# Performance work log

Measured on AMD Instinct MI355X. Metric: run time of the kernel, lower is better.

Reference implementation:

```python
import jax, jax.numpy as jnp
import numpy as np

N = 50000
E = 800000
IN_C, HID, OUT_C, HEADS = 128, 16, 64, 4
NEG_SLOPE = 0.2


def _gat_conv(x, src, dst, W, a_src, a_dst, b, heads, concat):
    # x: [N, Fin]; W: [Fin, heads*Fout]; a_src/a_dst: [heads, Fout]; b: [out]
    n = x.shape[0]
    h = (x @ W).reshape(n, heads, -1)                      # [N, H, F]
    alpha_s = jnp.einsum('nhf,hf->nh', h, a_src)           # [N, H]
    alpha_d = jnp.einsum('nhf,hf->nh', h, a_dst)
    e = jax.nn.leaky_relu(alpha_s[src] + alpha_d[dst], NEG_SLOPE)  # [E, H]
    m = jax.ops.segment_max(e, dst, num_segments=n)        # per-dest max (self-loops ensure nonempty)
    w = jnp.exp(e - m[dst])
    denom = jax.ops.segment_sum(w, dst, num_segments=n)
    alpha = w / (denom[dst] + 1e-16)                       # [E, H] segment softmax
    out = jax.ops.segment_sum(h[src] * alpha[:, :, None], dst, num_segments=n)  # [N, H, F]
    out = out.reshape(n, -1) if concat else out.mean(axis=1)
    return out + b


def setup_inputs() -> dict:
    key = jax.random.key(0)
    ks = jax.random.split(key, 16)
    x = jax.random.normal(ks[0], (N, IN_C), dtype=jnp.float32)
    edge_index = jax.random.randint(ks[1], (2, E), 0, N, dtype=jnp.int64)
    s = 0.1
    d = {'x': x, 'edge_index': edge_index}
    # layer 0: in=128 -> heads=4, F=16
    d['W0'] = jax.random.normal(ks[2], (IN_C, HEADS * HID), dtype=jnp.float32) * s
    d['as0'] = jax.random.normal(ks[3], (HEADS, HID), dtype=jnp.float32) * s
    d['ad0'] = jax.random.normal(ks[4], (HEADS, HID), dtype=jnp.float32) * s
    d['b0'] = jnp.zeros((HEADS * HID,), dtype=jnp.float32)
    # layer 1: in=64 -> heads=4, F=16
    d['W1'] = jax.random.normal(ks[5], (HEADS * HID, HEADS * HID), dtype=jnp.float32) * s
    d['as1'] = jax.random.normal(ks[6], (HEADS, HID), dtype=jnp.float32) * s
    d['ad1'] = jax.random.normal(ks[7], (HEADS, HID), dtype=jnp.float32) * s
    d['b1'] = jnp.zeros((HEADS * HID,), dtype=jnp.float32)
    # layer 2: in=64 -> heads=1, F=64, concat=False
    d['W2'] = jax.random.normal(ks[8], (HEADS * HID, OUT_C), dtype=jnp.float32) * s
    d['as2'] = jax.random.normal(ks[9], (1, OUT_C), dtype=jnp.float32) * s
    d['ad2'] = jax.random.normal(ks[10], (1, OUT_C), dtype=jnp.float32) * s
    d['b2'] = jnp.zeros((OUT_C,), dtype=jnp.float32)
    return d


def reference(x, edge_index, W0, as0, ad0, b0, W1, as1, ad1, b1, W2, as2, ad2, b2):
    loops = jnp.arange(N, dtype=edge_index.dtype)
    src = jnp.concatenate([edge_index[0], loops])  # PyG add_self_loops=True
    dst = jnp.concatenate([edge_index[1], loops])
    h = _gat_conv(x, src, dst, W0, as0, ad0, b0, HEADS, True)
    h = jax.nn.elu(h)
    h = _gat_conv(h, src, dst, W1, as1, ad1, b1, HEADS, True)
    h = jax.nn.elu(h)
    return _gat_conv(h, src, dst, W2, as2, ad2, b2, 1, False)
```

## Files before the change

### kernel.cpp

```cpp
#include <hip/hip_runtime.h>
#include <hip/hip_bf16.h>
#include <math.h>


#define NEG_SLOPE 0.2f
#define L1_CHUNK 4096


__global__ __launch_bounds__(256) void k_l1hist(
    const int* __restrict__ idx, int* __restrict__ ghist, int E, int etot) {
    __shared__ int h[256];
    const int t = threadIdx.x;
    h[t] = 0;
    __syncthreads();
    const int base = blockIdx.x * L1_CHUNK;
    for (int i = t; i < L1_CHUNK; i += 256) {
        int e = base + i;
        if (e >= etot) break;
        int dst = (e < E) ? idx[E + e] : (e - E);
        atomicAdd(&h[dst >> 8], 1);
    }
    __syncthreads();
    if (h[t]) atomicAdd(&ghist[t], h[t]);
}

__global__ __launch_bounds__(256) void k_scan256(
    const int* __restrict__ ghist, int* __restrict__ goff, int* __restrict__ gcur) {
    __shared__ int sc[256];
    const int t = threadIdx.x;
    int v = ghist[t];
    sc[t] = v;
    __syncthreads();
    for (int o = 1; o < 256; o <<= 1) {
        int x = (t >= o) ? sc[t - o] : 0;
        __syncthreads();
        sc[t] += x;
        __syncthreads();
    }
    int excl = sc[t] - v;
    goff[t] = excl;
    gcur[t] = excl;
    if (t == 255) goff[256] = sc[255];
}

__global__ __launch_bounds__(256) void k_l1scatter(
    const int* __restrict__ idx, int* __restrict__ gcur,
    unsigned long long* __restrict__ buf, int E, int etot) {
    __shared__ int h[256];
    __shared__ int lbase[256];
    const int t = threadIdx.x;
    h[t] = 0;
    __syncthreads();
    const int base = blockIdx.x * L1_CHUNK;
    for (int i = t; i < L1_CHUNK; i += 256) {
        int e = base + i;
        if (e >= etot) break;
        int dst = (e < E) ? idx[E + e] : (e - E);
        atomicAdd(&h[dst >> 8], 1);
    }
    __syncthreads();
    lbase[t] = h[t] ? atomicAdd(&gcur[t], h[t]) : 0;
    __syncthreads();
    h[t] = lbase[t];
    __syncthreads();
    for (int i = t; i < L1_CHUNK; i += 256) {
        int e = base + i;
        if (e >= etot) break;
        int dst, src;
        if (e < E) { dst = idx[E + e]; src = idx[e]; }
        else       { dst = src = e - E; }
        int pos = atomicAdd(&h[dst >> 8], 1);
        buf[pos] = ((unsigned long long)(unsigned)dst << 32) | (unsigned)src;
    }
}

__global__ __launch_bounds__(256) void k_l2build(
    const unsigned long long* __restrict__ buf, const int* __restrict__ goff,
    int* __restrict__ off, int* __restrict__ csr, int n, int etot) {
    __shared__ int sc[256];
    __shared__ int lcur[256];
    const int b = blockIdx.x, t = threadIdx.x;
    const int lo = goff[b], hi = goff[b + 1];
    sc[t] = 0;
    __syncthreads();
    for (int p = lo + t; p < hi; p += 256) {
        int dst = (int)(buf[p] >> 32);
        atomicAdd(&sc[dst & 255], 1);
    }
    __syncthreads();
    int v = sc[t];
    __syncthreads();
    sc[t] = v;
    __syncthreads();
    for (int o = 1; o < 256; o <<= 1) {
        int x = (t >= o) ? sc[t - o] : 0;
        __syncthreads();
        sc[t] += x;
        __syncthreads();
    }
    int excl = sc[t] - v;
    const int d = b * 256 + t;
    if (d < n) off[d] = lo + excl;
    lcur[t] = lo + excl;
    __syncthreads();
    for (int p = lo + t; p < hi; p += 256) {
        unsigned long long e = buf[p];
        int dst = (int)(e >> 32);
        int src = (int)(e & 0xffffffffu);
        int pos = atomicAdd(&lcur[dst & 255], 1);
        csr[pos] = src;
    }
    if (b == 0 && t == 0) off[n] = etot;
}


template <int H>
__device__ __forceinline__ float4 agg_node(
    const float* __restrict__ h, const float* __restrict__ asb,
    const float* __restrict__ adb, const int* __restrict__ off,
    const int* __restrict__ csr, int node, int q, int c4) {
    const int head = (H == 1) ? 0 : (c4 >> 2);
    const float ad_n = adb[node * H + head];
    const int b = off[node], e = off[node + 1];
    float den = 0.f;
    float4 acc = {0.f, 0.f, 0.f, 0.f};
    int p = b + q;
    int s_cur = 0; float as_cur = 0.f;
    if (p < e) { s_cur = csr[p]; as_cur = asb[s_cur * H + head]; }
    while (p < e) {
        const int pn = p + 4;
        int s_nxt = 0; float as_nxt = 0.f;
        if (pn < e) { s_nxt = csr[pn]; as_nxt = asb[s_nxt * H + head]; }
        float ev = as_cur + ad_n;
        ev = ev > 0.f ? ev : NEG_SLOPE * ev;
        float wv = __expf(ev);
        const float4 hv = *(const float4*)(h + (size_t)s_cur * 64 + c4 * 4);
        den += wv;
        acc.x = fmaf(wv, hv.x, acc.x);
        acc.y = fmaf(wv, hv.y, acc.y);
        acc.z = fmaf(wv, hv.z, acc.z);
        acc.w = fmaf(wv, hv.w, acc.w);
        p = pn; s_cur = s_nxt; as_cur = as_nxt;
    }
    den += __shfl_xor(den, 16); den += __shfl_xor(den, 32);
    acc.x += __shfl_xor(acc.x, 16); acc.x += __shfl_xor(acc.x, 32);
    acc.y += __shfl_xor(acc.y, 16); acc.y += __shfl_xor(acc.y, 32);
    acc.z += __shfl_xor(acc.z, 16); acc.z += __shfl_xor(acc.z, 32);
    acc.w += __shfl_xor(acc.w, 16); acc.w += __shfl_xor(acc.w, 32);
    float inv = 1.f / (den + 1e-16f);
    return make_float4(acc.x * inv, acc.y * inv, acc.z * inv, acc.w * inv);
}

template <int K, int H, int F>
__global__ __launch_bounds__(256) void k_gemm_alpha(
    const float* __restrict__ x, const float* __restrict__ W,
    const float* __restrict__ a_s, const float* __restrict__ a_d,
    float* __restrict__ h, float* __restrict__ as_o, float* __restrict__ ad_o,
    int n) {
    __shared__ float xs[16][K];
    const int tid = threadIdx.x;
    const int base = blockIdx.x * 16;
    int rows = n - base; if (rows > 16) rows = 16;
    const int kv = K / 4;
    for (int i = tid; i < rows * kv; i += 256) {
        int r = i / kv, c = i - r * kv;
        ((float4*)&xs[r][0])[c] = ((const float4*)(x + (size_t)(base + r) * K))[c];
    }
    __syncthreads();
    const int w = tid >> 6, lane = tid & 63;
    const int node0 = base + w * 4;
    float acc0 = 0.f, acc1 = 0.f, acc2 = 0.f, acc3 = 0.f;
    #pragma unroll 4
    for (int k = 0; k < K; ++k) {
        float wv = W[k * 64 + lane];
        acc0 = fmaf(xs[w * 4 + 0][k], wv, acc0);
        acc1 = fmaf(xs[w * 4 + 1][k], wv, acc1);
        acc2 = fmaf(xs[w * 4 + 2][k], wv, acc2);
        acc3 = fmaf(xs[w * 4 + 3][k], wv, acc3);
    }
    const int head = (H == 1) ? 0 : (lane >> 4);
    const int f = (H == 1) ? lane : (lane & (F - 1));
    const float asv = a_s[head * F + f];
    const float adv = a_d[head * F + f];
    float accs[4] = {acc0, acc1, acc2, acc3};
    #pragma unroll
    for (int j = 0; j < 4; ++j) {
        int node = node0 + j;
        if (node >= n) break;
        h[(size_t)node * 64 + lane] = accs[j];
        float vs = accs[j] * asv;
        float vd = accs[j] * adv;
        #pragma unroll
        for (int o = F >> 1; o > 0; o >>= 1) {
            vs += __shfl_xor(vs, o);
            vd += __shfl_xor(vd, o);
        }
        if (f == 0) {
            as_o[node * H + head] = vs;
            ad_o[node * H + head] = vd;
        }
    }
}

template <int HA, int HG, int FG>
__global__ __launch_bounds__(256) void k_agg_gemm(
    const float* __restrict__ h_in, const float* __restrict__ asb_in,
    const float* __restrict__ adb_in, const int* __restrict__ off,
    const int* __restrict__ csr, const float* __restrict__ bias,
    const float* __restrict__ W, const float* __restrict__ a_s,
    const float* __restrict__ a_d, float* __restrict__ h_out,
    float* __restrict__ asb_out, float* __restrict__ adb_out, int n) {
    __shared__ float xs[16][64];
    const int tid = threadIdx.x;
    const int w = tid >> 6, lane = tid & 63;
    const int q = lane >> 4, c4 = lane & 15;
    const int base = blockIdx.x * 16;
    #pragma unroll
    for (int j = 0; j < 4; ++j) {
        const int node = base + w * 4 + j;
        if (node < n) {
            float4 r = agg_node<HA>(h_in, asb_in, adb_in, off, csr, node, q, c4);
            if (q == 0) {
                r.x += bias[c4 * 4 + 0]; r.y += bias[c4 * 4 + 1];
                r.z += bias[c4 * 4 + 2]; r.w += bias[c4 * 4 + 3];
                r.x = r.x > 0.f ? r.x : expm1f(r.x);
                r.y = r.y > 0.f ? r.y : expm1f(r.y);
                r.z = r.z > 0.f ? r.z : expm1f(r.z);
                r.w = r.w > 0.f ? r.w : expm1f(r.w);
                *(float4*)&xs[w * 4 + j][c4 * 4] = r;
            }
        }
    }
    __syncthreads();
    float acc0 = 0.f, acc1 = 0.f, acc2 = 0.f, acc3 = 0.f;
    #pragma unroll 4
    for (int k = 0; k < 64; ++k) {
        float wv = W[k * 64 + lane];
        acc0 = fmaf(xs[w * 4 + 0][k], wv, acc0);
        acc1 = fmaf(xs[w * 4 + 1][k], wv, acc1);
        acc2 = fmaf(xs[w * 4 + 2][k], wv, acc2);
        acc3 = fmaf(xs[w * 4 + 3][k], wv, acc3);
    }
    const int head = (HG == 1) ? 0 : (lane >> 4);
    const int f = (HG == 1) ? lane : (lane & (FG - 1));
    const float asv = a_s[head * FG + f];
    const float adv = a_d[head * FG + f];
    float accs[4] = {acc0, acc1, acc2, acc3};
    const int node0 = base + w * 4;
    #pragma unroll
    for (int j = 0; j < 4; ++j) {
        int node = node0 + j;
        if (node >= n) break;
        h_out[(size_t)node * 64 + lane] = accs[j];
        float vs = accs[j] * asv;
        float vd = accs[j] * adv;
        #pragma unroll
        for (int o = FG >> 1; o > 0; o >>= 1) {
            vs += __shfl_xor(vs, o);
            vd += __shfl_xor(vd, o);
        }
        if (f == 0) {
            asb_out[node * HG + head] = vs;
            adb_out[node * HG + head] = vd;
        }
    }
}

__global__ __launch_bounds__(256) void k_agg_final(
    const float* __restrict__ h, const float* __restrict__ asb,
    const float* __restrict__ adb, const int* __restrict__ off,
    const int* __restrict__ csr, const float* __restrict__ bias,
    float* __restrict__ out, int n) {
    const int w = threadIdx.x >> 6, lane = threadIdx.x & 63;
    const int node = blockIdx.x * 4 + w;
    if (node >= n) return;
    const int q = lane >> 4, c4 = lane & 15;
    float4 r = agg_node<1>(h, asb, adb, off, csr, node, q, c4);
    if (q == 0) {
        r.x += bias[c4 * 4 + 0]; r.y += bias[c4 * 4 + 1];
        r.z += bias[c4 * 4 + 2]; r.w += bias[c4 * 4 + 3];
        *(float4*)(out + (size_t)node * 64 + c4 * 4) = r;
    }
}


extern "C" void kernel_launch(void* const* d_in, const int* in_sizes, int n_in,
                              void* d_out, int out_size, void* d_ws, size_t ws_size,
                              hipStream_t stream) {
    const float* x   = (const float*)d_in[0];
    const int*   idx = (const int*)d_in[1];
    const float* W0  = (const float*)d_in[2];
    const float* as0 = (const float*)d_in[3];
    const float* ad0 = (const float*)d_in[4];
    const float* b0  = (const float*)d_in[5];
    const float* W1  = (const float*)d_in[6];
    const float* as1 = (const float*)d_in[7];
    const float* ad1 = (const float*)d_in[8];
    const float* b1  = (const float*)d_in[9];
    const float* W2  = (const float*)d_in[10];
    const float* as2 = (const float*)d_in[11];
    const float* ad2 = (const float*)d_in[12];
    const float* b2  = (const float*)d_in[13];
    float* out = (float*)d_out;

    const int n    = in_sizes[0] / 128;
    const int E    = in_sizes[1] / 2;
    const int etot = E + n;

    char* p = (char*)d_ws;
    auto alloc = [&](size_t bytes) {
        char* r = p;
        p += (bytes + 255) & ~(size_t)255;
        return r;
    };
    int*   off   = (int*)alloc((size_t)(n + 1) * 4);
    int*   csr   = (int*)alloc((size_t)etot * 4);
    int*   ghist = (int*)alloc(256 * 4);
    int*   goff  = (int*)alloc(257 * 4);
    int*   gcur  = (int*)alloc(256 * 4);
    float* asbA  = (float*)alloc((size_t)n * 4 * 4);
    float* adbA  = (float*)alloc((size_t)n * 4 * 4);
    float* asbB  = (float*)alloc((size_t)n * 4 * 4);
    float* adbB  = (float*)alloc((size_t)n * 4 * 4);
    float* hA    = (float*)alloc((size_t)n * 64 * 4);
    float* hB    = (float*)alloc((size_t)n * 64 * 4);
    unsigned long long* buf = (unsigned long long*)hB;

    const int nb_l1 = (etot + L1_CHUNK - 1) / L1_CHUNK;
    const int nb_l2 = (n + 255) / 256;
    const int nb_g  = (n + 15) / 16;
    const int nb_w  = (n + 3) / 4;

    hipMemsetAsync(ghist, 0, 256 * 4, stream);
    k_l1hist<<<nb_l1, 256, 0, stream>>>(idx, ghist, E, etot);
    k_scan256<<<1, 256, 0, stream>>>(ghist, goff, gcur);
    k_l1scatter<<<nb_l1, 256, 0, stream>>>(idx, gcur, buf, E, etot);
    k_l2build<<<nb_l2, 256, 0, stream>>>(buf, goff, off, csr, n, etot);

    k_gemm_alpha<128, 4, 16><<<nb_g, 256, 0, stream>>>(x, W0, as0, ad0, hA, asbA, adbA, n);
    k_agg_gemm<4, 4, 16><<<nb_g, 256, 0, stream>>>(hA, asbA, adbA, off, csr, b0,
                                                   W1, as1, ad1, hB, asbB, adbB, n);
    k_agg_gemm<4, 1, 64><<<nb_g, 256, 0, stream>>>(hB, asbB, adbB, off, csr, b1,
                                                   W2, as2, ad2, hA, asbA, adbA, n);
    k_agg_final<<<nb_w, 256, 0, stream>>>(hA, asbA, adbA, off, csr, b2, out, n);
}
```

Measured before the change: 302.5 us.

## Precompute per-edge attention weights in separate kernels before aggregation

Adds a destination array to the CSR build and a new per-edge kernel that computes exp(leaky_relu(as[src]+ad[dst])) for all heads into an edge-weight buffer before each aggregation. The aggregation loop then reads a contiguous weight instead of doing a dependent gather of as[src] and an exp per lane, which removes one random gather from the critical chain. In exchange it adds three extra kernel launches, extra global traffic for the weight buffer (etot*16 bytes written and read per layer) and an extra dst array, and the CSR scratch buffer now aliases the weight buffer.

```diff
diff --git a/kernel.cpp b/kernel.cpp
--- a/kernel.cpp
+++ b/kernel.cpp
@@ -76,7 +76,8 @@
 
 __global__ __launch_bounds__(256) void k_l2build(
     const unsigned long long* __restrict__ buf, const int* __restrict__ goff,
-    int* __restrict__ off, int* __restrict__ csr, int n, int etot) {
+    int* __restrict__ off, int* __restrict__ csr, int* __restrict__ dstarr,
+    int n, int etot) {
     __shared__ int sc[256];
     __shared__ int lcur[256];
     const int b = blockIdx.x, t = threadIdx.x;
@@ -109,38 +110,64 @@
         int src = (int)(e & 0xffffffffu);
         int pos = atomicAdd(&lcur[dst & 255], 1);
         csr[pos] = src;
+        dstarr[pos] = dst;
     }
     if (b == 0 && t == 0) off[n] = etot;
+}
+
+
+template <int H>
+__global__ __launch_bounds__(256) void k_weights(
+    const int* __restrict__ csr, const int* __restrict__ dstarr,
+    const float* __restrict__ asb, const float* __restrict__ adb,
+    float* __restrict__ wE, int etot) {
+    int p = blockIdx.x * 256 + threadIdx.x;
+    if (p >= etot) return;
+    int s = csr[p], d = dstarr[p];
+    if (H == 4) {
+        float4 a = *(const float4*)(asb + (size_t)s * 4);
+        float4 b = *(const float4*)(adb + (size_t)d * 4);
+        float4 ev;
+        ev.x = a.x + b.x; ev.y = a.y + b.y; ev.z = a.z + b.z; ev.w = a.w + b.w;
+        ev.x = ev.x > 0.f ? ev.x : NEG_SLOPE * ev.x;
+        ev.y = ev.y > 0.f ? ev.y : NEG_SLOPE * ev.y;
+        ev.z = ev.z > 0.f ? ev.z : NEG_SLOPE * ev.z;
+        ev.w = ev.w > 0.f ? ev.w : NEG_SLOPE * ev.w;
+        ev.x = __expf(ev.x); ev.y = __expf(ev.y);
+        ev.z = __expf(ev.z); ev.w = __expf(ev.w);
+        *(float4*)(wE + (size_t)p * 4) = ev;
+    } else {
+        float ev = asb[s] + adb[d];
+        ev = ev > 0.f ? ev : NEG_SLOPE * ev;
+        wE[p] = __expf(ev);
+    }
 }
 
 
 template <int H>
 __device__ __forceinline__ float4 agg_node(
-    const float* __restrict__ h, const float* __restrict__ asb,
-    const float* __restrict__ adb, const int* __restrict__ off,
-    const int* __restrict__ csr, int node, int q, int c4) {
+    const float* __restrict__ h, const float* __restrict__ wE,
+    const int* __restrict__ off, const int* __restrict__ csr,
+    int node, int q, int c4) {
     const int head = (H == 1) ? 0 : (c4 >> 2);
-    const float ad_n = adb[node * H + head];
     const int b = off[node], e = off[node + 1];
     float den = 0.f;
     float4 acc = {0.f, 0.f, 0.f, 0.f};
     int p = b + q;
-    int s_cur = 0; float as_cur = 0.f;
-    if (p < e) { s_cur = csr[p]; as_cur = asb[s_cur * H + head]; }
+    int s0 = 0;
+    if (p < e) s0 = csr[p];
     while (p < e) {
         const int pn = p + 4;
-        int s_nxt = 0; float as_nxt = 0.f;
-        if (pn < e) { s_nxt = csr[pn]; as_nxt = asb[s_nxt * H + head]; }
-        float ev = as_cur + ad_n;
-        ev = ev > 0.f ? ev : NEG_SLOPE * ev;
-        float wv = __expf(ev);
-        const float4 hv = *(const float4*)(h + (size_t)s_cur * 64 + c4 * 4);
+        int s1 = 0;
+        if (pn < e) s1 = csr[pn];
+        float wv = (H == 1) ? wE[p] : wE[(size_t)p * 4 + head];
+        const float4 hv = *(const float4*)(h + (size_t)s0 * 64 + c4 * 4);
         den += wv;
         acc.x = fmaf(wv, hv.x, acc.x);
         acc.y = fmaf(wv, hv.y, acc.y);
         acc.z = fmaf(wv, hv.z, acc.z);
         acc.w = fmaf(wv, hv.w, acc.w);
-        p = pn; s_cur = s_nxt; as_cur = as_nxt;
+        p = pn; s0 = s1;
     }
     den += __shfl_xor(den, 16); den += __shfl_xor(den, 32);
     acc.x += __shfl_xor(acc.x, 16); acc.x += __shfl_xor(acc.x, 32);
@@ -204,12 +231,12 @@
 
 template <int HA, int HG, int FG>
 __global__ __launch_bounds__(256) void k_agg_gemm(
-    const float* __restrict__ h_in, const float* __restrict__ asb_in,
-    const float* __restrict__ adb_in, const int* __restrict__ off,
-    const int* __restrict__ csr, const float* __restrict__ bias,
-    const float* __restrict__ W, const float* __restrict__ a_s,
-    const float* __restrict__ a_d, float* __restrict__ h_out,
-    float* __restrict__ asb_out, float* __restrict__ adb_out, int n) {
+    const float* __restrict__ h_in, const float* __restrict__ wE,
+    const int* __restrict__ off, const int* __restrict__ csr,
+    const float* __restrict__ bias, const float* __restrict__ W,
+    const float* __restrict__ a_s, const float* __restrict__ a_d,
+    float* __restrict__ h_out, float* __restrict__ asb_out,
+    float* __restrict__ adb_out, int n) {
     __shared__ float xs[16][64];
     const int tid = threadIdx.x;
     const int w = tid >> 6, lane = tid & 63;
@@ -219,7 +246,7 @@
     for (int j = 0; j < 4; ++j) {
         const int node = base + w * 4 + j;
         if (node < n) {
-            float4 r = agg_node<HA>(h_in, asb_in, adb_in, off, csr, node, q, c4);
+            float4 r = agg_node<HA>(h_in, wE, off, csr, node, q, c4);
             if (q == 0) {
                 r.x += bias[c4 * 4 + 0]; r.y += bias[c4 * 4 + 1];
                 r.z += bias[c4 * 4 + 2]; r.w += bias[c4 * 4 + 3];
@@ -267,15 +294,14 @@
 }
 
 __global__ __launch_bounds__(256) void k_agg_final(
-    const float* __restrict__ h, const float* __restrict__ asb,
-    const float* __restrict__ adb, const int* __restrict__ off,
-    const int* __restrict__ csr, const float* __restrict__ bias,
-    float* __restrict__ out, int n) {
+    const float* __restrict__ h, const float* __restrict__ wE,
+    const int* __restrict__ off, const int* __restrict__ csr,
+    const float* __restrict__ bias, float* __restrict__ out, int n) {
     const int w = threadIdx.x >> 6, lane = threadIdx.x & 63;
     const int node = blockIdx.x * 4 + w;
     if (node >= n) return;
     const int q = lane >> 4, c4 = lane & 15;
-    float4 r = agg_node<1>(h, asb, adb, off, csr, node, q, c4);
+    float4 r = agg_node<1>(h, wE, off, csr, node, q, c4);
     if (q == 0) {
         r.x += bias[c4 * 4 + 0]; r.y += bias[c4 * 4 + 1];
         r.z += bias[c4 * 4 + 2]; r.w += bias[c4 * 4 + 3];
@@ -313,21 +339,24 @@
         p += (bytes + 255) & ~(size_t)255;
         return r;
     };
-    int*   off   = (int*)alloc((size_t)(n + 1) * 4);
-    int*   csr   = (int*)alloc((size_t)etot * 4);
-    int*   ghist = (int*)alloc(256 * 4);
-    int*   goff  = (int*)alloc(257 * 4);
-    int*   gcur  = (int*)alloc(256 * 4);
-    float* asbA  = (float*)alloc((size_t)n * 4 * 4);
-    float* adbA  = (float*)alloc((size_t)n * 4 * 4);
-    float* asbB  = (float*)alloc((size_t)n * 4 * 4);
-    float* adbB  = (float*)alloc((size_t)n * 4 * 4);
-    float* hA    = (float*)alloc((size_t)n * 64 * 4);
-    float* hB    = (float*)alloc((size_t)n * 64 * 4);
-    unsigned long long* buf = (unsigned long long*)hB;
+    int*   off    = (int*)alloc((size_t)(n + 1) * 4);
+    int*   csr    = (int*)alloc((size_t)etot * 4);
+    int*   dstarr = (int*)alloc((size_t)etot * 4);
+    int*   ghist  = (int*)alloc(256 * 4);
+    int*   goff   = (int*)alloc(257 * 4);
+    int*   gcur   = (int*)alloc(256 * 4);
+    float* asbA   = (float*)alloc((size_t)n * 4 * 4);
+    float* adbA   = (float*)alloc((size_t)n * 4 * 4);
+    float* asbB   = (float*)alloc((size_t)n * 4 * 4);
+    float* adbB   = (float*)alloc((size_t)n * 4 * 4);
+    float* hA     = (float*)alloc((size_t)n * 64 * 4);
+    float* hB     = (float*)alloc((size_t)n * 64 * 4);
+    float* wE     = (float*)alloc((size_t)etot * 4 * 4);
+    unsigned long long* buf = (unsigned long long*)wE;
 
     const int nb_l1 = (etot + L1_CHUNK - 1) / L1_CHUNK;
     const int nb_l2 = (n + 255) / 256;
+    const int nb_e  = (etot + 255) / 256;
     const int nb_g  = (n + 15) / 16;
     const int nb_w  = (n + 3) / 4;
 
@@ -335,12 +364,15 @@
     k_l1hist<<<nb_l1, 256, 0, stream>>>(idx, ghist, E, etot);
     k_scan256<<<1, 256, 0, stream>>>(ghist, goff, gcur);
     k_l1scatter<<<nb_l1, 256, 0, stream>>>(idx, gcur, buf, E, etot);
-    k_l2build<<<nb_l2, 256, 0, stream>>>(buf, goff, off, csr, n, etot);
+    k_l2build<<<nb_l2, 256, 0, stream>>>(buf, goff, off, csr, dstarr, n, etot);
 
     k_gemm_alpha<128, 4, 16><<<nb_g, 256, 0, stream>>>(x, W0, as0, ad0, hA, asbA, adbA, n);
-    k_agg_gemm<4, 4, 16><<<nb_g, 256, 0, stream>>>(hA, asbA, adbA, off, csr, b0,
+    k_weights<4><<<nb_e, 256, 0, stream>>>(csr, dstarr, asbA, adbA, wE, etot);
+    k_agg_gemm<4, 4, 16><<<nb_g, 256, 0, stream>>>(hA, wE, off, csr, b0,
                                                    W1, as1, ad1, hB, asbB, adbB, n);
-    k_agg_gemm<4, 1, 64><<<nb_g, 256, 0, stream>>>(hB, asbB, adbB, off, csr, b1,
+    k_weights<4><<<nb_e, 256, 0, stream>>>(csr, dstarr, asbB, adbB, wE, etot);
+    k_agg_gemm<4, 1, 64><<<nb_g, 256, 0, stream>>>(hB, wE, off, csr, b1,
                                                    W2, as2, ad2, hA, asbA, adbA, n);
-    k_agg_final<<<nb_w, 256, 0, stream>>>(hA, asbA, adbA, off, csr, b2, out, n);
-}
+    k_weights<1><<<nb_e, 256, 0, stream>>>(csr, dstarr, asbA, adbA, wE, etot);
+    k_agg_final<<<nb_w, 256, 0, stream>>>(hA, wE, off, csr, b2, out, n);
+}
```

After: 322.7 us. +6.7%, slower.

## Interleave edge gathers of four nodes per wavefront in aggregation

Applied to the files above, without the earlier changes.

The aggregation helper now processes four destination nodes at once per wavefront, issuing the CSR, alpha and feature gathers for all four together so more independent memory loads are in flight. This replaces the per-node loop with one-step software prefetch. The final aggregation kernel moves from one node per wave to four nodes per wave with fewer blocks. The cost is lanes idling when degrees differ, since the loop runs to the maximum degree of the four nodes, plus extra register pressure.

```diff
diff --git a/kernel.cpp b/kernel.cpp
--- a/kernel.cpp
+++ b/kernel.cpp
@@ -115,40 +115,67 @@
 
 
 template <int H>
-__device__ __forceinline__ float4 agg_node(
+__device__ __forceinline__ void agg_node4(
     const float* __restrict__ h, const float* __restrict__ asb,
     const float* __restrict__ adb, const int* __restrict__ off,
-    const int* __restrict__ csr, int node, int q, int c4) {
+    const int* __restrict__ csr, int node0, int n, int q, int c4,
+    float4* res) {
     const int head = (H == 1) ? 0 : (c4 >> 2);
-    const float ad_n = adb[node * H + head];
-    const int b = off[node], e = off[node + 1];
-    float den = 0.f;
-    float4 acc = {0.f, 0.f, 0.f, 0.f};
-    int p = b + q;
-    int s_cur = 0; float as_cur = 0.f;
-    if (p < e) { s_cur = csr[p]; as_cur = asb[s_cur * H + head]; }
-    while (p < e) {
-        const int pn = p + 4;
-        int s_nxt = 0; float as_nxt = 0.f;
-        if (pn < e) { s_nxt = csr[pn]; as_nxt = asb[s_nxt * H + head]; }
-        float ev = as_cur + ad_n;
-        ev = ev > 0.f ? ev : NEG_SLOPE * ev;
-        float wv = __expf(ev);
-        const float4 hv = *(const float4*)(h + (size_t)s_cur * 64 + c4 * 4);
-        den += wv;
-        acc.x = fmaf(wv, hv.x, acc.x);
-        acc.y = fmaf(wv, hv.y, acc.y);
-        acc.z = fmaf(wv, hv.z, acc.z);
-        acc.w = fmaf(wv, hv.w, acc.w);
-        p = pn; s_cur = s_nxt; as_cur = as_nxt;
-    }
-    den += __shfl_xor(den, 16); den += __shfl_xor(den, 32);
-    acc.x += __shfl_xor(acc.x, 16); acc.x += __shfl_xor(acc.x, 32);
-    acc.y += __shfl_xor(acc.y, 16); acc.y += __shfl_xor(acc.y, 32);
-    acc.z += __shfl_xor(acc.z, 16); acc.z += __shfl_xor(acc.z, 32);
-    acc.w += __shfl_xor(acc.w, 16); acc.w += __shfl_xor(acc.w, 32);
-    float inv = 1.f / (den + 1e-16f);
-    return make_float4(acc.x * inv, acc.y * inv, acc.z * inv, acc.w * inv);
+    float den[4] = {0.f, 0.f, 0.f, 0.f};
+    float4 acc[4];
+    int p[4], e[4];
+    float adn[4];
+    #pragma unroll
+    for (int j = 0; j < 4; ++j) {
+        acc[j] = make_float4(0.f, 0.f, 0.f, 0.f);
+        const int node = node0 + j;
+        if (node < n) {
+            p[j] = off[node] + q;
+            e[j] = off[node + 1];
+            adn[j] = adb[node * H + head];
+        } else {
+            p[j] = 0; e[j] = 0; adn[j] = 0.f;
+        }
+    }
+    while (p[0] < e[0] || p[1] < e[1] || p[2] < e[2] || p[3] < e[3]) {
+        int s[4]; bool valid[4];
+        #pragma unroll
+        for (int j = 0; j < 4; ++j) {
+            valid[j] = p[j] < e[j];
+            s[j] = csr[valid[j] ? p[j] : 0];
+        }
+        float as_[4];
+        #pragma unroll
+        for (int j = 0; j < 4; ++j) as_[j] = asb[s[j] * H + head];
+        float4 hv[4];
+        #pragma unroll
+        for (int j = 0; j < 4; ++j)
+            hv[j] = *(const float4*)(h + (size_t)s[j] * 64 + c4 * 4);
+        #pragma unroll
+        for (int j = 0; j < 4; ++j) {
+            float ev = as_[j] + adn[j];
+            ev = ev > 0.f ? ev : NEG_SLOPE * ev;
+            float wv = valid[j] ? __expf(ev) : 0.f;
+            den[j] += wv;
+            acc[j].x = fmaf(wv, hv[j].x, acc[j].x);
+            acc[j].y = fmaf(wv, hv[j].y, acc[j].y);
+            acc[j].z = fmaf(wv, hv[j].z, acc[j].z);
+            acc[j].w = fmaf(wv, hv[j].w, acc[j].w);
+            p[j] += 4;
+        }
+    }
+    #pragma unroll
+    for (int j = 0; j < 4; ++j) {
+        float d = den[j];
+        float4 a = acc[j];
+        d += __shfl_xor(d, 16); d += __shfl_xor(d, 32);
+        a.x += __shfl_xor(a.x, 16); a.x += __shfl_xor(a.x, 32);
+        a.y += __shfl_xor(a.y, 16); a.y += __shfl_xor(a.y, 32);
+        a.z += __shfl_xor(a.z, 16); a.z += __shfl_xor(a.z, 32);
+        a.w += __shfl_xor(a.w, 16); a.w += __shfl_xor(a.w, 32);
+        float inv = 1.f / (d + 1e-16f);
+        res[j] = make_float4(a.x * inv, a.y * inv, a.z * inv, a.w * inv);
+    }
 }
 
 template <int K, int H, int F>
@@ -215,12 +242,13 @@
     const int w = tid >> 6, lane = tid & 63;
     const int q = lane >> 4, c4 = lane & 15;
     const int base = blockIdx.x * 16;
-    #pragma unroll
-    for (int j = 0; j < 4; ++j) {
-        const int node = base + w * 4 + j;
-        if (node < n) {
-            float4 r = agg_node<HA>(h_in, asb_in, adb_in, off, csr, node, q, c4);
-            if (q == 0) {
+    float4 res[4];
+    agg_node4<HA>(h_in, asb_in, adb_in, off, csr, base + w * 4, n, q, c4, res);
+    if (q == 0) {
+        #pragma unroll
+        for (int j = 0; j < 4; ++j) {
+            if (base + w * 4 + j < n) {
+                float4 r = res[j];
                 r.x += bias[c4 * 4 + 0]; r.y += bias[c4 * 4 + 1];
                 r.z += bias[c4 * 4 + 2]; r.w += bias[c4 * 4 + 3];
                 r.x = r.x > 0.f ? r.x : expm1f(r.x);
@@ -271,15 +299,23 @@
     const float* __restrict__ adb, const int* __restrict__ off,
     const int* __restrict__ csr, const float* __restrict__ bias,
     float* __restrict__ out, int n) {
-    const int w = threadIdx.x >> 6, lane = threadIdx.x & 63;
-    const int node = blockIdx.x * 4 + w;
-    if (node >= n) return;
+    const int tid = threadIdx.x;
+    const int w = tid >> 6, lane = tid & 63;
     const int q = lane >> 4, c4 = lane & 15;
-    float4 r = agg_node<1>(h, asb, adb, off, csr, node, q, c4);
+    const int base = blockIdx.x * 16;
+    float4 res[4];
+    agg_node4<1>(h, asb, adb, off, csr, base + w * 4, n, q, c4, res);
     if (q == 0) {
-        r.x += bias[c4 * 4 + 0]; r.y += bias[c4 * 4 + 1];
-        r.z += bias[c4 * 4 + 2]; r.w += bias[c4 * 4 + 3];
-        *(float4*)(out + (size_t)node * 64 + c4 * 4) = r;
+        #pragma unroll
+        for (int j = 0; j < 4; ++j) {
+            const int node = base + w * 4 + j;
+            if (node < n) {
+                float4 r = res[j];
+                r.x += bias[c4 * 4 + 0]; r.y += bias[c4 * 4 + 1];
+                r.z += bias[c4 * 4 + 2]; r.w += bias[c4 * 4 + 3];
+                *(float4*)(out + (size_t)node * 64 + c4 * 4) = r;
+            }
+        }
     }
 }
 
@@ -329,7 +365,6 @@
     const int nb_l1 = (etot + L1_CHUNK - 1) / L1_CHUNK;
     const int nb_l2 = (n + 255) / 256;
     const int nb_g  = (n + 15) / 16;
-    const int nb_w  = (n + 3) / 4;
 
     hipMemsetAsync(ghist, 0, 256 * 4, stream);
     k_l1hist<<<nb_l1, 256, 0, stream>>>(idx, ghist, E, etot);
@@ -342,5 +377,5 @@
                                                    W1, as1, ad1, hB, asbB, adbB, n);
     k_agg_gemm<4, 1, 64><<<nb_g, 256, 0, stream>>>(hB, asbB, adbB, off, csr, b1,
                                                    W2, as2, ad2, hA, asbA, adbA, n);
-    k_agg_final<<<nb_w, 256, 0, stream>>>(hA, asbA, adbA, off, csr, b2, out, n);
-}
+    k_agg_final<<<nb_g, 256, 0, stream>>>(hA, asbA, adbA, off, csr, b2, out, n);
+}
```

Result: no change. 297.1 us (-1.8%).

## Assign one node per quarter-wave in aggregation and precompute per-chunk scatter bases

Applied to the files above, without the earlier changes.

Aggregation now gives each 16-lane quarter of a wavefront its own destination node, which walks all of that node's edges sequentially with a two-deep software prefetch of source index, attention logit and feature row. This replaces the previous scheme where four quarters split one node's edges and combined them with cross-lane shuffles. The intent is to drop those shuffle reductions and get more independent nodes in flight. The cost is wave divergence on skewed degrees, since the loop runs until every quarter finishes. Separately, the CSR build writes per-chunk histograms and a column scan computes each chunk's bucket bases. This removes the memset, the global atomics and the second histogram pass from the scatter kernel, but the single-block scan now loops serially over all chunks.

```diff
diff --git a/kernel.cpp b/kernel.cpp
--- a/kernel.cpp
+++ b/kernel.cpp
@@ -8,7 +8,7 @@
 
 
 __global__ __launch_bounds__(256) void k_l1hist(
-    const int* __restrict__ idx, int* __restrict__ ghist, int E, int etot) {
+    const int* __restrict__ idx, int* __restrict__ bh, int E, int etot) {
     __shared__ int h[256];
     const int t = threadIdx.x;
     h[t] = 0;
@@ -21,55 +21,48 @@
         atomicAdd(&h[dst >> 8], 1);
     }
     __syncthreads();
-    if (h[t]) atomicAdd(&ghist[t], h[t]);
-}
-
-__global__ __launch_bounds__(256) void k_scan256(
-    const int* __restrict__ ghist, int* __restrict__ goff, int* __restrict__ gcur) {
+    bh[blockIdx.x * 256 + t] = h[t];
+}
+
+__global__ __launch_bounds__(256) void k_colscan(
+    const int* __restrict__ bh, int* __restrict__ base,
+    int* __restrict__ goff, int nchunk) {
     __shared__ int sc[256];
     const int t = threadIdx.x;
-    int v = ghist[t];
-    sc[t] = v;
+    int tot = 0;
+    for (int r = 0; r < nchunk; ++r) tot += bh[r * 256 + t];
+    sc[t] = tot;
     __syncthreads();
     for (int o = 1; o < 256; o <<= 1) {
-        int x = (t >= o) ? sc[t - o] : 0;
+        int v = (t >= o) ? sc[t - o] : 0;
         __syncthreads();
-        sc[t] += x;
+        sc[t] += v;
         __syncthreads();
     }
-    int excl = sc[t] - v;
-    goff[t] = excl;
-    gcur[t] = excl;
+    int run = sc[t] - tot;
+    goff[t] = run;
     if (t == 255) goff[256] = sc[255];
+    for (int r = 0; r < nchunk; ++r) {
+        base[r * 256 + t] = run;
+        run += bh[r * 256 + t];
+    }
 }
 
 __global__ __launch_bounds__(256) void k_l1scatter(
-    const int* __restrict__ idx, int* __restrict__ gcur,
+    const int* __restrict__ idx, const int* __restrict__ base,
     unsigned long long* __restrict__ buf, int E, int etot) {
-    __shared__ int h[256];
-    __shared__ int lbase[256];
+    __shared__ int cur[256];
     const int t = threadIdx.x;
-    h[t] = 0;
-    __syncthreads();
-    const int base = blockIdx.x * L1_CHUNK;
+    cur[t] = base[blockIdx.x * 256 + t];
+    __syncthreads();
+    const int cb = blockIdx.x * L1_CHUNK;
     for (int i = t; i < L1_CHUNK; i += 256) {
-        int e = base + i;
-        if (e >= etot) break;
-        int dst = (e < E) ? idx[E + e] : (e - E);
-        atomicAdd(&h[dst >> 8], 1);
-    }
-    __syncthreads();
-    lbase[t] = h[t] ? atomicAdd(&gcur[t], h[t]) : 0;
-    __syncthreads();
-    h[t] = lbase[t];
-    __syncthreads();
-    for (int i = t; i < L1_CHUNK; i += 256) {
-        int e = base + i;
+        int e = cb + i;
         if (e >= etot) break;
         int dst, src;
         if (e < E) { dst = idx[E + e]; src = idx[e]; }
         else       { dst = src = e - E; }
-        int pos = atomicAdd(&h[dst >> 8], 1);
+        int pos = atomicAdd(&cur[dst >> 8], 1);
         buf[pos] = ((unsigned long long)(unsigned)dst << 32) | (unsigned)src;
     }
 }
@@ -115,39 +108,42 @@
 
 
 template <int H>
-__device__ __forceinline__ float4 agg_node(
+__device__ __forceinline__ float4 aggq(
     const float* __restrict__ h, const float* __restrict__ asb,
     const float* __restrict__ adb, const int* __restrict__ off,
-    const int* __restrict__ csr, int node, int q, int c4) {
+    const int* __restrict__ csr, int node, int c4, int n) {
     const int head = (H == 1) ? 0 : (c4 >> 2);
-    const float ad_n = adb[node * H + head];
-    const int b = off[node], e = off[node + 1];
     float den = 0.f;
-    float4 acc = {0.f, 0.f, 0.f, 0.f};
-    int p = b + q;
-    int s_cur = 0; float as_cur = 0.f;
-    if (p < e) { s_cur = csr[p]; as_cur = asb[s_cur * H + head]; }
-    while (p < e) {
-        const int pn = p + 4;
-        int s_nxt = 0; float as_nxt = 0.f;
-        if (pn < e) { s_nxt = csr[pn]; as_nxt = asb[s_nxt * H + head]; }
-        float ev = as_cur + ad_n;
+    float4 acc = make_float4(0.f, 0.f, 0.f, 0.f);
+    int p = 0, e = 0;
+    float adn = 0.f;
+    if (node < n) {
+        p = off[node];
+        e = off[node + 1];
+        adn = adb[node * H + head];
+    }
+    int s0 = csr[p < e ? p : 0];
+    int s1 = csr[(p + 1) < e ? (p + 1) : 0];
+    float as0 = asb[s0 * H + head];
+    float4 hv0 = *(const float4*)(h + (size_t)s0 * 64 + c4 * 4);
+    while (__any(p < e)) {
+        const bool valid = p < e;
+        const int p2 = p + 2;
+        const int s2 = csr[p2 < e ? p2 : 0];
+        const float as1 = asb[s1 * H + head];
+        const float4 hv1 = *(const float4*)(h + (size_t)s1 * 64 + c4 * 4);
+        float ev = as0 + adn;
         ev = ev > 0.f ? ev : NEG_SLOPE * ev;
-        float wv = __expf(ev);
-        const float4 hv = *(const float4*)(h + (size_t)s_cur * 64 + c4 * 4);
+        const float wv = valid ? __expf(ev) : 0.f;
         den += wv;
-        acc.x = fmaf(wv, hv.x, acc.x);
-        acc.y = fmaf(wv, hv.y, acc.y);
-        acc.z = fmaf(wv, hv.z, acc.z);
-        acc.w = fmaf(wv, hv.w, acc.w);
-        p = pn; s_cur = s_nxt; as_cur = as_nxt;
-    }
-    den += __shfl_xor(den, 16); den += __shfl_xor(den, 32);
-    acc.x += __shfl_xor(acc.x, 16); acc.x += __shfl_xor(acc.x, 32);
-    acc.y += __shfl_xor(acc.y, 16); acc.y += __shfl_xor(acc.y, 32);
-    acc.z += __shfl_xor(acc.z, 16); acc.z += __shfl_xor(acc.z, 32);
-    acc.w += __shfl_xor(acc.w, 16); acc.w += __shfl_xor(acc.w, 32);
-    float inv = 1.f / (den + 1e-16f);
+        acc.x = fmaf(wv, hv0.x, acc.x);
+        acc.y = fmaf(wv, hv0.y, acc.y);
+        acc.z = fmaf(wv, hv0.z, acc.z);
+        acc.w = fmaf(wv, hv0.w, acc.w);
+        p = p + 1;
+        s0 = s1; s1 = s2; as0 = as1; hv0 = hv1;
+    }
+    const float inv = 1.f / (den + 1e-16f);
     return make_float4(acc.x * inv, acc.y * inv, acc.z * inv, acc.w * inv);
 }
 
@@ -215,21 +211,16 @@
     const int w = tid >> 6, lane = tid & 63;
     const int q = lane >> 4, c4 = lane & 15;
     const int base = blockIdx.x * 16;
-    #pragma unroll
-    for (int j = 0; j < 4; ++j) {
-        const int node = base + w * 4 + j;
-        if (node < n) {
-            float4 r = agg_node<HA>(h_in, asb_in, adb_in, off, csr, node, q, c4);
-            if (q == 0) {
-                r.x += bias[c4 * 4 + 0]; r.y += bias[c4 * 4 + 1];
-                r.z += bias[c4 * 4 + 2]; r.w += bias[c4 * 4 + 3];
-                r.x = r.x > 0.f ? r.x : expm1f(r.x);
-                r.y = r.y > 0.f ? r.y : expm1f(r.y);
-                r.z = r.z > 0.f ? r.z : expm1f(r.z);
-                r.w = r.w > 0.f ? r.w : expm1f(r.w);
-                *(float4*)&xs[w * 4 + j][c4 * 4] = r;
-            }
-        }
+    const int nodeA = base + w * 4 + q;
+    float4 r = aggq<HA>(h_in, asb_in, adb_in, off, csr, nodeA, c4, n);
+    if (nodeA < n) {
+        const float4 bv = *(const float4*)(bias + c4 * 4);
+        r.x += bv.x; r.y += bv.y; r.z += bv.z; r.w += bv.w;
+        r.x = r.x > 0.f ? r.x : expm1f(r.x);
+        r.y = r.y > 0.f ? r.y : expm1f(r.y);
+        r.z = r.z > 0.f ? r.z : expm1f(r.z);
+        r.w = r.w > 0.f ? r.w : expm1f(r.w);
+        *(float4*)&xs[w * 4 + q][c4 * 4] = r;
     }
     __syncthreads();
     float acc0 = 0.f, acc1 = 0.f, acc2 = 0.f, acc3 = 0.f;
@@ -271,14 +262,14 @@
     const float* __restrict__ adb, const int* __restrict__ off,
     const int* __restrict__ csr, const float* __restrict__ bias,
     float* __restrict__ out, int n) {
-    const int w = threadIdx.x >> 6, lane = threadIdx.x & 63;
-    const int node = blockIdx.x * 4 + w;
-    if (node >= n) return;
+    const int tid = threadIdx.x;
+    const int w = tid >> 6, lane = tid & 63;
     const int q = lane >> 4, c4 = lane & 15;
-    float4 r = agg_node<1>(h, asb, adb, off, csr, node, q, c4);
-    if (q == 0) {
-        r.x += bias[c4 * 4 + 0]; r.y += bias[c4 * 4 + 1];
-        r.z += bias[c4 * 4 + 2]; r.w += bias[c4 * 4 + 3];
+    const int node = blockIdx.x * 16 + w * 4 + q;
+    float4 r = aggq<1>(h, asb, adb, off, csr, node, c4, n);
+    if (node < n) {
+        const float4 bv = *(const float4*)(bias + c4 * 4);
+        r.x += bv.x; r.y += bv.y; r.z += bv.z; r.w += bv.w;
         *(float4*)(out + (size_t)node * 64 + c4 * 4) = r;
     }
 }
@@ -313,28 +304,26 @@
         p += (bytes + 255) & ~(size_t)255;
         return r;
     };
-    int*   off   = (int*)alloc((size_t)(n + 1) * 4);
-    int*   csr   = (int*)alloc((size_t)etot * 4);
-    int*   ghist = (int*)alloc(256 * 4);
-    int*   goff  = (int*)alloc(257 * 4);
-    int*   gcur  = (int*)alloc(256 * 4);
-    float* asbA  = (float*)alloc((size_t)n * 4 * 4);
-    float* adbA  = (float*)alloc((size_t)n * 4 * 4);
-    float* asbB  = (float*)alloc((size_t)n * 4 * 4);
-    float* adbB  = (float*)alloc((size_t)n * 4 * 4);
-    float* hA    = (float*)alloc((size_t)n * 64 * 4);
-    float* hB    = (float*)alloc((size_t)n * 64 * 4);
+    const int nb_l1 = (etot + L1_CHUNK - 1) / L1_CHUNK;
+    int*   off  = (int*)alloc((size_t)(n + 1) * 4);
+    int*   csr  = (int*)alloc((size_t)etot * 4);
+    int*   bh   = (int*)alloc((size_t)nb_l1 * 256 * 4);
+    int*   base = (int*)alloc((size_t)nb_l1 * 256 * 4);
+    int*   goff = (int*)alloc(257 * 4);
+    float* asbA = (float*)alloc((size_t)n * 4 * 4);
+    float* adbA = (float*)alloc((size_t)n * 4 * 4);
+    float* asbB = (float*)alloc((size_t)n * 4 * 4);
+    float* adbB = (float*)alloc((size_t)n * 4 * 4);
+    float* hA   = (float*)alloc((size_t)n * 64 * 4);
+    float* hB   = (float*)alloc((size_t)n * 64 * 4);
     unsigned long long* buf = (unsigned long long*)hB;
 
-    const int nb_l1 = (etot + L1_CHUNK - 1) / L1_CHUNK;
     const int nb_l2 = (n + 255) / 256;
     const int nb_g  = (n + 15) / 16;
-    const int nb_w  = (n + 3) / 4;
-
-    hipMemsetAsync(ghist, 0, 256 * 4, stream);
-    k_l1hist<<<nb_l1, 256, 0, stream>>>(idx, ghist, E, etot);
-    k_scan256<<<1, 256, 0, stream>>>(ghist, goff, gcur);
-    k_l1scatter<<<nb_l1, 256, 0, stream>>>(idx, gcur, buf, E, etot);
+
+    k_l1hist<<<nb_l1, 256, 0, stream>>>(idx, bh, E, etot);
+    k_colscan<<<1, 256, 0, stream>>>(bh, base, goff, nb_l1);
+    k_l1scatter<<<nb_l1, 256, 0, stream>>>(idx, base, buf, E, etot);
     k_l2build<<<nb_l2, 256, 0, stream>>>(buf, goff, off, csr, n, etot);
 
     k_gemm_alpha<128, 4, 16><<<nb_g, 256, 0, stream>>>(x, W0, as0, ad0, hA, asbA, adbA, n);
@@ -342,5 +331,5 @@
                                                    W1, as1, ad1, hB, asbB, adbB, n);
     k_agg_gemm<4, 1, 64><<<nb_g, 256, 0, stream>>>(hB, asbB, adbB, off, csr, b1,
                                                    W2, as2, ad2, hA, asbA, adbA, n);
-    k_agg_final<<<nb_w, 256, 0, stream>>>(hA, asbA, adbA, off, csr, b2, out, n);
-}
+    k_agg_final<<<nb_g, 256, 0, stream>>>(hA, asbA, adbA, off, csr, b2, out, n);
+}
```

Result: slower. 343.1 us (+13.4%).
